# Performance work log

Hardware: AMD Instinct MI355X
Metric: run time of the kernel (lower is better)

Reference implementation:

```python
import jax, jax.numpy as jnp
import numpy as np
import math

N_COARSE, N_FINE = 8192, 32768
DEC_DIM, ENC_DIM, OUT_DIM, K = 256, 128, 128, 16
LN_EPS = 1e-5


def setup_inputs() -> dict:
    key = jax.random.key(0)
    ks = jax.random.split(key, 16)
    s = lambda fan_in: 1.0 / math.sqrt(fan_in)
    return {
        "decoder_features": jax.random.normal(ks[0], (N_COARSE, DEC_DIM), jnp.float32),
        "decoder_pos": jax.random.normal(ks[1], (N_COARSE, 3), jnp.float32),
        "encoder_features": jax.random.normal(ks[2], (N_FINE, ENC_DIM), jnp.float32),
        "encoder_pos": jax.random.normal(ks[3], (N_FINE, 3), jnp.float32),
        "encoder_labels": jax.random.randint(ks[4], (N_FINE,), 0, 13, jnp.int64),
        # params (torch nn.Linear default init scale)
        "Wq": jax.random.uniform(ks[5], (DEC_DIM, ENC_DIM), jnp.float32, -s(ENC_DIM), s(ENC_DIM)),
        "bq": jnp.zeros((DEC_DIM,), jnp.float32),
        "Wk": jax.random.uniform(ks[6], (DEC_DIM, DEC_DIM), jnp.float32, -s(DEC_DIM), s(DEC_DIM)),
        "bk": jnp.zeros((DEC_DIM,), jnp.float32),
        "Wv": jax.random.uniform(ks[7], (DEC_DIM, DEC_DIM), jnp.float32, -s(DEC_DIM), s(DEC_DIM)),
        "bv": jnp.zeros((DEC_DIM,), jnp.float32),
        "W1": jax.random.uniform(ks[8], (OUT_DIM, DEC_DIM + ENC_DIM), jnp.float32, -s(DEC_DIM + ENC_DIM), s(DEC_DIM + ENC_DIM)),
        "b1": jnp.zeros((OUT_DIM,), jnp.float32),
        "W2": jax.random.uniform(ks[9], (OUT_DIM, OUT_DIM), jnp.float32, -s(OUT_DIM), s(OUT_DIM)),
        "b2": jnp.zeros((OUT_DIM,), jnp.float32),
        "ln_g": jnp.ones((OUT_DIM,), jnp.float32),
        "ln_b": jnp.zeros((OUT_DIM,), jnp.float32),
    }


def _knn_indices(encoder_pos, decoder_pos, k):
    # For each fine (encoder) point, k nearest coarse (decoder) points.
    # squared distances [N_fine, N_coarse]
    d2 = (
        jnp.sum(encoder_pos * encoder_pos, axis=1, keepdims=True)
        - 2.0 * encoder_pos @ decoder_pos.T
        + jnp.sum(decoder_pos * decoder_pos, axis=1)[None, :]
    )
    _, idx = jax.lax.top_k(-d2, k)  # [N_fine, K]
    return idx


def reference(decoder_features, decoder_pos, encoder_features, encoder_pos,
              encoder_labels, Wq, bq, Wk, bk, Wv, bv, W1, b1, W2, b2, ln_g, ln_b):
    idx = _knn_indices(encoder_pos, decoder_pos, K)            # [Nf, K]
    nbr = decoder_features[idx]                                 # [Nf, K, Dd]
    query = encoder_features @ Wq.T + bq                        # [Nf, Dd]
    keys = nbr @ Wk.T + bk                                      # [Nf, K, Dd]
    values = nbr @ Wv.T + bv                                    # [Nf, K, Dd]
    scores = jnp.einsum('nd,nkd->nk', query, keys) / math.sqrt(DEC_DIM)
    # segment softmax over edges grouped by fine target == softmax over K
    weights = jax.nn.softmax(scores, axis=-1)                   # [Nf, K]
    agg = jnp.einsum('nk,nkd->nd', weights, values)             # [Nf, Dd]
    combined = jnp.concatenate([agg, encoder_features], axis=-1)
    h = jax.nn.relu(combined @ W1.T + b1)
    up = h @ W2.T + b2                                          # [Nf, out]
    mu = jnp.mean(up, axis=-1, keepdims=True)
    var = jnp.var(up, axis=-1, keepdims=True)
    out = (up - mu) * jax.lax.rsqrt(var + LN_EPS) * ln_g + ln_b
    # dropout is identity in eval mode
    return (out, encoder_pos, encoder_labels)
```

## Files before the change

kernel.cpp:

```cpp
#include <hip/hip_runtime.h>
#include <hip/hip_bf16.h>

typedef __hip_bfloat16 bf16;
typedef unsigned short u16;
typedef float f32x2 __attribute__((ext_vector_type(2)));

#define NC 8192
#define NF 32768
#define KNN 16
#define FMAXV 3.402823466e+38f

__device__ __forceinline__ float bfbits2f(u16 u){
  union { unsigned u; float f; } x; x.u = ((unsigned)u) << 16; return x.f;
}
__device__ __forceinline__ float asfloat(unsigned u){
  union { unsigned u; float f; } x; x.u = u; return x.f;
}
__device__ __forceinline__ f32x2 pk_fma(f32x2 a, f32x2 b, f32x2 c){
  f32x2 d;
  asm("v_pk_fma_f32 %0, %1, %2, %3" : "=v"(d) : "v"(a), "v"(b), "v"(c));
  return d;
}

__global__ __launch_bounds__(256) void k_prep(const float* __restrict__ dpos,
                                              const float* __restrict__ W1,
                                              const float* __restrict__ W2,
                                              float4* __restrict__ posP,
                                              float4* __restrict__ W1eSa,
                                              float4* __restrict__ W1eSb,
                                              float4* __restrict__ W2Sa,
                                              float4* __restrict__ W2Sb){
  int g = blockIdx.x * 256 + threadIdx.x;
  if (g < 4096){
    const float2* dp2 = (const float2*)(dpos + (size_t)g * 6);
    float2 a = dp2[0], b = dp2[1], c = dp2[2];
    float x0 = a.x, y0 = a.y, z0 = b.x;
    float x1 = b.y, y1 = c.x, z1 = c.y;
    float dd0 = __fadd_rn(__fadd_rn(__fmul_rn(x0,x0), __fmul_rn(y0,y0)), __fmul_rn(z0,z0));
    float dd1 = __fadd_rn(__fadd_rn(__fmul_rn(x1,x1), __fmul_rn(y1,y1)), __fmul_rn(z1,z1));
    posP[g * 2]     = make_float4(x0, x1, y0, y1);
    posP[g * 2 + 1] = make_float4(z0, z1, dd0 * 0.5f, dd1 * 0.5f);
  } else if (g >= 8192 && g < 10240){
    int f = g - 8192; int c4 = f >> 6, jg = f & 63;
    W1eSa[f] = ((const float4*)(W1 + (size_t)(2 * jg) * 384 + 256))[c4];
  } else if (g >= 10240 && g < 12288){
    int f = g - 10240; int c4 = f >> 6, jg = f & 63;
    W1eSb[f] = ((const float4*)(W1 + (size_t)(2 * jg + 1) * 384 + 256))[c4];
  } else if (g >= 12288 && g < 14336){
    int f = g - 12288; int c4 = f >> 6, jg = f & 63;
    W2Sa[f] = ((const float4*)(W2 + (size_t)(2 * jg) * 128))[c4];
  } else if (g >= 14336){
    int f = g - 14336; int c4 = f >> 6, jg = f & 63;
    W2Sb[f] = ((const float4*)(W2 + (size_t)(2 * jg + 1) * 128))[c4];
  }
}

__global__ __launch_bounds__(256) void k_wprod(const float* __restrict__ Wk,
                                               const float* __restrict__ Wv,
                                               const float* __restrict__ Wq,
                                               const float* __restrict__ W1,
                                               const float* __restrict__ bk,
                                               const float* __restrict__ bv,
                                               const float* __restrict__ bq,
                                               float* __restrict__ WkqS,
                                               float* __restrict__ WvuS,
                                               float* __restrict__ bkq,
                                               float* __restrict__ bvu,
                                               float* __restrict__ wbq,
                                               float* __restrict__ sbq){
  __shared__ float red[256];
  int b = blockIdx.x, t = threadIdx.x;
  if (b < 128){
    int c = b;
    float acc = 0.f;
    for (int j = 0; j < 256; ++j)
      acc = fmaf(Wk[(size_t)j * 256 + t], Wq[(size_t)j * 128 + c], acc);
    WkqS[(size_t)((t >> 2) * 128 + c) * 4 + (t & 3)] = acc;
    red[t] = bk[t] * Wq[(size_t)t * 128 + c];
    __syncthreads();
    for (int s = 128; s > 0; s >>= 1){ if (t < s) red[t] += red[t + s]; __syncthreads(); }
    if (t == 0) bkq[c] = red[0];
  } else if (b < 256){
    int h = b - 128;
    float acc = 0.f;
    for (int c2 = 0; c2 < 256; ++c2)
      acc = fmaf(Wv[(size_t)c2 * 256 + t], W1[(size_t)h * 384 + c2], acc);
    WvuS[(size_t)((t >> 2) * 128 + h) * 4 + (t & 3)] = acc;
    red[t] = bv[t] * W1[(size_t)h * 384 + t];
    __syncthreads();
    for (int s = 128; s > 0; s >>= 1){ if (t < s) red[t] += red[t + s]; __syncthreads(); }
    if (t == 0) bvu[h] = red[0];
  } else {
    float acc = 0.f;
    for (int j = 0; j < 256; ++j)
      acc = fmaf(Wk[(size_t)j * 256 + t], bq[j], acc);
    wbq[t] = acc;
    red[t] = bk[t] * bq[t];
    __syncthreads();
    for (int s = 128; s > 0; s >>= 1){ if (t < s) red[t] += red[t + s]; __syncthreads(); }
    if (t == 0) sbq[0] = red[0];
  }
}

__global__ __launch_bounds__(256) void k_dec(const float* __restrict__ df,
                                             const float4* __restrict__ WkqS,
                                             const float4* __restrict__ WvuS,
                                             const float* __restrict__ bkq,
                                             const float* __restrict__ bvu,
                                             const float* __restrict__ wbq,
                                             const float* __restrict__ sbq,
                                             bf16* __restrict__ Zd, bf16* __restrict__ Ud,
                                             float* __restrict__ bqK){
  __shared__ float part[16][16];
  int t = threadIdx.x;
  int g0 = blockIdx.x * 16;
  int half = __builtin_amdgcn_readfirstlane(t >> 7);
  int c = t & 127;
  const float4* W = half ? WvuS : WkqS;
  float acc[16];
  #pragma unroll
  for (int p = 0; p < 16; ++p) acc[p] = 0.f;
  for (int j4 = 0; j4 < 64; ++j4){
    float4 w = W[j4 * 128 + c];
    #pragma unroll
    for (int p = 0; p < 16; ++p){
      float4 a = ((const float4*)(df + (size_t)(g0 + p) * 256))[j4];
      acc[p] += w.x*a.x + w.y*a.y + w.z*a.z + w.w*a.w;
    }
  }
  float bias = half ? bvu[c] : bkq[c];
  bf16* dst = half ? Ud : Zd;
  #pragma unroll
  for (int p = 0; p < 16; ++p)
    dst[(size_t)(g0 + p) * 128 + c] = __float2bfloat16(acc[p] + bias);
  {
    int r = t >> 4, seg = t & 15;
    float s = 0.f;
    const float* dr = df + (size_t)(g0 + r) * 256 + seg * 16;
    const float* wq = wbq + seg * 16;
    #pragma unroll
    for (int e = 0; e < 16; ++e) s = fmaf(dr[e], wq[e], s);
    part[r][seg] = s;
  }
  __syncthreads();
  if (t < 16){
    float s = sbq[0];
    #pragma unroll
    for (int seg = 0; seg < 16; ++seg) s += part[t][seg];
    bqK[g0 + t] = s;
  }
}

__global__ __launch_bounds__(256) void k_attn(const float* __restrict__ epos,
                                              const float4* __restrict__ posP,
                                              const float* __restrict__ ef,
                                              const bf16* __restrict__ Zd,
                                              const bf16* __restrict__ Ud,
                                              const float* __restrict__ bqK,
                                              bf16* __restrict__ hagg){
  __shared__ float smin[8 * 64];
  __shared__ float tauLDS[8];
  __shared__ int   cnt[8];
  __shared__ float lval[8][64];
  __shared__ int   lidx[8][64];

  int t = threadIdx.x, lane = t & 63, w = t >> 6;
  int n0 = blockIdx.x * 8;
  f32x2 nex2[8], ney2[8], nez2[8];
  #pragma unroll
  for (int p = 0; p < 8; ++p){
    float nx = -epos[(n0 + p) * 3 + 0];
    float ny = -epos[(n0 + p) * 3 + 1];
    float nz = -epos[(n0 + p) * 3 + 2];
    nex2[p].x = nx; nex2[p].y = nx;
    ney2[p].x = ny; ney2[p].y = ny;
    nez2[p].x = nz; nez2[p].y = nz;
  }
  const float4* base = posP + w * 2048;

  f32x2 vmin2[8];
  #pragma unroll
  for (int p = 0; p < 8; ++p){ vmin2[p].x = FMAXV; vmin2[p].y = FMAXV; }
  #pragma unroll 2
  for (int s = 0; s < 16; ++s){
    int q2 = (s * 64 + lane) * 2;
    float4 XY = base[q2], ZW = base[q2 + 1];
    f32x2 X = {XY.x, XY.y}, Y = {XY.z, XY.w}, Z = {ZW.x, ZW.y}, W = {ZW.z, ZW.w};
    #pragma unroll
    for (int p = 0; p < 8; ++p){
      f32x2 v2 = pk_fma(nex2[p], X, W);
      v2 = pk_fma(ney2[p], Y, v2);
      v2 = pk_fma(nez2[p], Z, v2);
      vmin2[p].x = fminf(vmin2[p].x, v2.x);
      vmin2[p].y = fminf(vmin2[p].y, v2.y);
    }
  }
  float vmin[8];
  #pragma unroll
  for (int p = 0; p < 8; ++p) vmin[p] = fminf(vmin2[p].x, vmin2[p].y);

  #pragma unroll
  for (int k = 2; k <= 64; k <<= 1){
    #pragma unroll
    for (int j = k >> 1; j > 0; j >>= 1){
      bool keepmin = ((lane & j) == 0) == ((lane & k) == 0);
      #pragma unroll
      for (int p = 0; p < 8; ++p){
        float pv = __shfl_xor(vmin[p], j);
        vmin[p] = keepmin ? fminf(vmin[p], pv) : fmaxf(vmin[p], pv);
      }
    }
  }
  if (lane < 16){
    #pragma unroll
    for (int p = 0; p < 8; ++p) smin[p * 64 + w * 16 + lane] = vmin[p];
  }
  if (t < 8) cnt[t] = 0;
  __syncthreads();
  #pragma unroll
  for (int u = 0; u < 2; ++u){
    int p = w * 2 + u;
    float v = smin[p * 64 + lane];
    #pragma unroll
    for (int k = 2; k <= 64; k <<= 1){
      #pragma unroll
      for (int j = k >> 1; j > 0; j >>= 1){
        float pv = __shfl_xor(v, j);
        bool keepmin = ((lane & j) == 0) == ((lane & k) == 0);
        v = keepmin ? fminf(v, pv) : fmaxf(v, pv);
      }
    }
    if (lane == 16) tauLDS[p] = v;
  }
  __syncthreads();
  float tau0[8];
  #pragma unroll
  for (int p = 0; p < 8; ++p) tau0[p] = tauLDS[p];

  #pragma unroll 2
  for (int s = 0; s < 16; ++s){
    int q = s * 64 + lane;
    float4 XY = base[q * 2], ZW = base[q * 2 + 1];
    f32x2 X = {XY.x, XY.y}, Y = {XY.z, XY.w}, Z = {ZW.x, ZW.y}, W = {ZW.z, ZW.w};
    int cand0 = w * 2048 + q * 2;
    #pragma unroll
    for (int p = 0; p < 8; ++p){
      f32x2 v2 = pk_fma(nex2[p], X, W);
      v2 = pk_fma(ney2[p], Y, v2);
      v2 = pk_fma(nez2[p], Z, v2);
      if (v2.x <= tau0[p]){
        int slot = atomicAdd(&cnt[p], 1);
        if (slot < 64){ lval[p][slot] = v2.x; lidx[p][slot] = cand0; }
      }
      if (v2.y <= tau0[p]){
        int slot = atomicAdd(&cnt[p], 1);
        if (slot < 64){ lval[p][slot] = v2.y; lidx[p][slot] = cand0 + 1; }
      }
    }
  }
  __syncthreads();

  for (int u = 0; u < 2; ++u){
    int p = w * 2 + u;
    int n = n0 + p;
    int c = cnt[p]; if (c > 64) c = 64;
    float v  = (lane < c) ? lval[p][lane] : FMAXV;
    int   id = (lane < c) ? lidx[p][lane] : 0x7fffffff;
    #pragma unroll
    for (int k = 2; k <= 64; k <<= 1){
      #pragma unroll
      for (int j = k >> 1; j > 0; j >>= 1){
        float pv  = __shfl_xor(v, j);
        int   pid = __shfl_xor(id, j);
        bool keepmin = ((lane & j) == 0) == ((lane & k) == 0);
        bool pless = (pv < v) || (pv == v && pid < id);
        bool take = keepmin ? pless : !pless;
        if (take){ v = pv; id = pid; }
      }
    }
    int topi = id;

    *(float2*)&smin[w * 128 + lane * 2] = *(const float2*)(ef + (size_t)n * 128 + lane * 2);
    asm volatile("s_waitcnt lgkmcnt(0)" ::: "memory");

    int kk = lane & 15, part = lane >> 4;
    int ik = __shfl(topi, kk);
    const uint4*  zr = (const uint4*)((const u16*)Zd + (size_t)ik * 128) + part * 4;
    const float4* e4 = (const float4*)(smin + w * 128) + part * 8;
    float pr = 0.f;
    #pragma unroll
    for (int i = 0; i < 4; ++i){
      uint4 z = zr[i];
      float4 ea = e4[2 * i], eb = e4[2 * i + 1];
      pr = fmaf(ea.x, asfloat(z.x << 16), pr); pr = fmaf(ea.y, asfloat(z.x & 0xffff0000u), pr);
      pr = fmaf(ea.z, asfloat(z.y << 16), pr); pr = fmaf(ea.w, asfloat(z.y & 0xffff0000u), pr);
      pr = fmaf(eb.x, asfloat(z.z << 16), pr); pr = fmaf(eb.y, asfloat(z.z & 0xffff0000u), pr);
      pr = fmaf(eb.z, asfloat(z.w << 16), pr); pr = fmaf(eb.w, asfloat(z.w & 0xffff0000u), pr);
    }
    pr += __shfl_xor(pr, 16);
    pr += __shfl_xor(pr, 32);
    float sc = (pr + bqK[ik]) * (1.0f / 16.0f);

    float mx = sc;
    #pragma unroll
    for (int off = 8; off >= 1; off >>= 1) mx = fmaxf(mx, __shfl_xor(mx, off));
    float e = (lane < KNN) ? __expf(sc - mx) : 0.f;
    float l = e;
    #pragma unroll
    for (int off = 8; off >= 1; off >>= 1) l += __shfl_xor(l, off);
    float wgt = (lane < KNN) ? (e / l) : 0.f;

    float a0 = 0.f, a1 = 0.f;
    #pragma unroll
    for (int k = 0; k < KNN; ++k){
      int ikk = __shfl(topi, k);
      float wk = __shfl(wgt, k);
      ushort2 uu = *(const ushort2*)((const u16*)Ud + (size_t)ikk * 128 + lane * 2);
      a0 = fmaf(wk, bfbits2f(uu.x), a0);
      a1 = fmaf(wk, bfbits2f(uu.y), a1);
    }
    bf16 h0 = __float2bfloat16(a0), h1 = __float2bfloat16(a1);
    ushort2 st; st.x = *(u16*)&h0; st.y = *(u16*)&h1;
    *(ushort2*)(hagg + (size_t)n * 128 + lane * 2) = st;
  }
}

__global__ __launch_bounds__(256) void k_mlp(const bf16* __restrict__ hagg,
                                             const float* __restrict__ ef,
                                             const float4* __restrict__ W1eSa,
                                             const float4* __restrict__ W1eSb,
                                             const float* __restrict__ b1,
                                             const float4* __restrict__ W2Sa,
                                             const float4* __restrict__ W2Sb,
                                             const float* __restrict__ b2,
                                             const float* __restrict__ lng, const float* __restrict__ lnb,
                                             const float* __restrict__ epos, const int* __restrict__ lab,
                                             float* __restrict__ out){
  __shared__ float hbuf[16 * 128];
  __shared__ float ubuf[16 * 128];
  __shared__ float stats[32];
  int t = threadIdx.x;
  int n0 = blockIdx.x * 16;
  {
    int gid = blockIdx.x * 256 + t;
    if (gid < NF){
      float* op = out + (size_t)NF * 128;
      op[gid * 3 + 0] = epos[gid * 3 + 0];
      op[gid * 3 + 1] = epos[gid * 3 + 1];
      op[gid * 3 + 2] = epos[gid * 3 + 2];
      out[(size_t)NF * 128 + (size_t)NF * 3 + gid] = (float)lab[gid];
    }
  }
  int jg = t & 63;
  int pg4 = __builtin_amdgcn_readfirstlane((t >> 6) * 4);
  int j0 = jg * 2;
  float acc[2][4];
  #pragma unroll
  for (int a = 0; a < 2; ++a)
    #pragma unroll
    for (int p = 0; p < 4; ++p) acc[a][p] = 0.f;
  for (int c4 = 0; c4 < 32; ++c4){
    float4 wa = W1eSa[c4 * 64 + jg];
    float4 wb = W1eSb[c4 * 64 + jg];
    #pragma unroll
    for (int p = 0; p < 4; ++p){
      float4 x = ((const float4*)(ef + (size_t)(n0 + pg4 + p) * 128))[c4];
      acc[0][p] += wa.x*x.x + wa.y*x.y + wa.z*x.z + wa.w*x.w;
      acc[1][p] += wb.x*x.x + wb.y*x.y + wb.z*x.z + wb.w*x.w;
    }
  }
  float b1a = b1[j0], b1b = b1[j0 + 1];
  #pragma unroll
  for (int p = 0; p < 4; ++p){
    size_t row = (size_t)(n0 + pg4 + p);
    ushort2 hgv = *(const ushort2*)((const u16*)hagg + row * 128 + j0);
    hbuf[(pg4 + p) * 128 + j0]     = fmaxf(acc[0][p] + b1a + bfbits2f(hgv.x), 0.f);
    hbuf[(pg4 + p) * 128 + j0 + 1] = fmaxf(acc[1][p] + b1b + bfbits2f(hgv.y), 0.f);
  }
  __syncthreads();
  float acc2[2][4];
  #pragma unroll
  for (int a = 0; a < 2; ++a)
    #pragma unroll
    for (int p = 0; p < 4; ++p) acc2[a][p] = 0.f;
  const float4* hb4 = (const float4*)hbuf;
  for (int c4 = 0; c4 < 32; ++c4){
    float4 wa = W2Sa[c4 * 64 + jg];
    float4 wb = W2Sb[c4 * 64 + jg];
    #pragma unroll
    for (int p = 0; p < 4; ++p){
      float4 x = hb4[(pg4 + p) * 32 + c4];
      acc2[0][p] += wa.x*x.x + wa.y*x.y + wa.z*x.z + wa.w*x.w;
      acc2[1][p] += wb.x*x.x + wb.y*x.y + wb.z*x.z + wb.w*x.w;
    }
  }
  float b2a = b2[j0], b2b = b2[j0 + 1];
  float u[2][4];
  #pragma unroll
  for (int p = 0; p < 4; ++p){
    u[0][p] = acc2[0][p] + b2a;
    u[1][p] = acc2[1][p] + b2b;
    ubuf[(pg4 + p) * 128 + j0]     = u[0][p];
    ubuf[(pg4 + p) * 128 + j0 + 1] = u[1][p];
  }
  __syncthreads();
  {
    int p = t >> 4, qi = t & 15;
    const float* ub = &ubuf[p * 128 + qi * 8];
    float s = 0.f, s2 = 0.f;
    #pragma unroll
    for (int e2i = 0; e2i < 8; ++e2i){ float v = ub[e2i]; s += v; s2 += v * v; }
    #pragma unroll
    for (int off = 1; off < 16; off <<= 1){ s += __shfl_xor(s, off); s2 += __shfl_xor(s2, off); }
    if (qi == 0){
      float mu = s * (1.f / 128.f);
      float var = s2 * (1.f / 128.f) - mu * mu;
      stats[p] = mu;
      stats[16 + p] = rsqrtf(fmaxf(var, 0.f) + 1e-5f);
    }
  }
  __syncthreads();
  float ga = lng[j0], gb = lng[j0 + 1];
  float ba = lnb[j0], bbv = lnb[j0 + 1];
  #pragma unroll
  for (int p = 0; p < 4; ++p){
    float mu = stats[pg4 + p], rs = stats[16 + pg4 + p];
    out[(size_t)(n0 + pg4 + p) * 128 + j0]     = (u[0][p] - mu) * rs * ga + ba;
    out[(size_t)(n0 + pg4 + p) * 128 + j0 + 1] = (u[1][p] - mu) * rs * gb + bbv;
  }
}

extern "C" void kernel_launch(void* const* d_in, const int* in_sizes, int n_in,
                              void* d_out, int out_size, void* d_ws, size_t ws_size,
                              hipStream_t stream){
  const float* df   = (const float*)d_in[0];
  const float* dpos = (const float*)d_in[1];
  const float* ef   = (const float*)d_in[2];
  const float* epos = (const float*)d_in[3];
  const int*   lab  = (const int*)d_in[4];
  const float* Wq = (const float*)d_in[5];
  const float* bq = (const float*)d_in[6];
  const float* Wk = (const float*)d_in[7];
  const float* bk = (const float*)d_in[8];
  const float* Wv = (const float*)d_in[9];
  const float* bv = (const float*)d_in[10];
  const float* W1 = (const float*)d_in[11];
  const float* b1 = (const float*)d_in[12];
  const float* W2 = (const float*)d_in[13];
  const float* b2 = (const float*)d_in[14];
  const float* lng = (const float*)d_in[15];
  const float* lnb = (const float*)d_in[16];
  float* out = (float*)d_out;

  char* wsb = (char*)d_ws;
  float4* posP  = (float4*)(wsb);
  bf16*   Zd    = (bf16*)(wsb + 131072);
  bf16*   Ud    = (bf16*)(wsb + 2228224);
  float*  bqK   = (float*)(wsb + 4325376);
  bf16*   hagg  = (bf16*)(wsb + 4358144);
  float4* W1eSa = (float4*)(wsb + 12746752);
  float4* W1eSb = (float4*)(wsb + 12779520);
  float4* W2Sa  = (float4*)(wsb + 12812288);
  float4* W2Sb  = (float4*)(wsb + 12845056);
  float*  WkqS  = (float*)(wsb + 12877824);
  float*  WvuS  = (float*)(wsb + 13008896);
  float*  bkq   = (float*)(wsb + 13139968);
  float*  bvu   = (float*)(wsb + 13140480);
  float*  wbq   = (float*)(wsb + 13140992);
  float*  sbq   = (float*)(wsb + 13142016);

  k_prep  <<<64,  256, 0, stream>>>(dpos, W1, W2, posP, W1eSa, W1eSb, W2Sa, W2Sb);
  k_wprod <<<257, 256, 0, stream>>>(Wk, Wv, Wq, W1, bk, bv, bq, WkqS, WvuS, bkq, bvu, wbq, sbq);
  k_dec   <<<NC / 16, 256, 0, stream>>>(df, (const float4*)WkqS, (const float4*)WvuS, bkq, bvu, wbq, sbq, Zd, Ud, bqK);
  k_attn  <<<NF / 8, 256, 0, stream>>>(epos, posP, ef, Zd, Ud, bqK, hagg);
  k_mlp   <<<NF / 16, 256, 0, stream>>>(hagg, ef, W1eSa, W1eSb, b1, W2Sa, W2Sb, b2, lng, lnb, epos, lab, out);
  (void)in_sizes; (void)n_in; (void)out_size; (void)ws_size;
}
```

Before: 335.2 us.

## Interleave two query points per wave and shorten bitonic sorts in kNN kernel

Processes the two query points per wave together instead of in a sequential loop, interleaving shuffles, loads and FMAs to expose more instruction-level parallelism. The threshold selection builds a bitonic sequence from two pre-sorted 16-runs by mirrored indexing, so only merge stages are needed. The top-16 selection uses sort-16 then min-merge steps instead of a full 64-wide sort. The encoder feature row is read directly from global memory rather than staged through LDS. This raises register pressure and relies on the partial-sort logic being correct.

```diff
diff --git a/kernel.cpp b/kernel.cpp
--- a/kernel.cpp
+++ b/kernel.cpp
@@ -217,20 +217,24 @@
   }
   if (t < 8) cnt[t] = 0;
   __syncthreads();
-  #pragma unroll
-  for (int u = 0; u < 2; ++u){
-    int p = w * 2 + u;
-    float v = smin[p * 64 + lane];
-    #pragma unroll
-    for (int k = 2; k <= 64; k <<= 1){
-      #pragma unroll
-      for (int j = k >> 1; j > 0; j >>= 1){
-        float pv = __shfl_xor(v, j);
-        bool keepmin = ((lane & j) == 0) == ((lane & k) == 0);
-        v = keepmin ? fminf(v, pv) : fmaxf(v, pv);
-      }
-    }
-    if (lane == 16) tauLDS[p] = v;
+
+  {
+    int src = (lane & 16) ? (lane ^ 15) : lane;
+    float v0 = smin[(w * 2 + 0) * 64 + src];
+    float v1 = smin[(w * 2 + 1) * 64 + src];
+    #pragma unroll
+    for (int j = 16; j > 0; j >>= 1){
+      bool keepmin = ((lane & 32) == 0) == ((lane & j) == 0);
+      float p0 = __shfl_xor(v0, j); v0 = keepmin ? fminf(v0, p0) : fmaxf(v0, p0);
+      float p1 = __shfl_xor(v1, j); v1 = keepmin ? fminf(v1, p1) : fmaxf(v1, p1);
+    }
+    #pragma unroll
+    for (int j = 32; j > 0; j >>= 1){
+      bool keepmin = ((lane & j) == 0);
+      float p0 = __shfl_xor(v0, j); v0 = keepmin ? fminf(v0, p0) : fmaxf(v0, p0);
+      float p1 = __shfl_xor(v1, j); v1 = keepmin ? fminf(v1, p1) : fmaxf(v1, p1);
+    }
+    if (lane == 16){ tauLDS[w * 2] = v0; tauLDS[w * 2 + 1] = v1; }
   }
   __syncthreads();
   float tau0[8];
@@ -260,68 +264,113 @@
   }
   __syncthreads();
 
-  for (int u = 0; u < 2; ++u){
-    int p = w * 2 + u;
-    int n = n0 + p;
-    int c = cnt[p]; if (c > 64) c = 64;
-    float v  = (lane < c) ? lval[p][lane] : FMAXV;
-    int   id = (lane < c) ? lidx[p][lane] : 0x7fffffff;
-    #pragma unroll
-    for (int k = 2; k <= 64; k <<= 1){
+  {
+    int p0 = w * 2, p1 = w * 2 + 1;
+    int nA = n0 + p0, nB = n0 + p1;
+    int c0 = cnt[p0]; if (c0 > 64) c0 = 64;
+    int c1 = cnt[p1]; if (c1 > 64) c1 = 64;
+    float va = (lane < c0) ? lval[p0][lane] : FMAXV;
+    int   ia = (lane < c0) ? lidx[p0][lane] : 0x7fffffff;
+    float vb = (lane < c1) ? lval[p1][lane] : FMAXV;
+    int   ib = (lane < c1) ? lidx[p1][lane] : 0x7fffffff;
+
+    #pragma unroll
+    for (int k = 2; k <= 16; k <<= 1){
       #pragma unroll
       for (int j = k >> 1; j > 0; j >>= 1){
-        float pv  = __shfl_xor(v, j);
-        int   pid = __shfl_xor(id, j);
-        bool keepmin = ((lane & j) == 0) == ((lane & k) == 0);
-        bool pless = (pv < v) || (pv == v && pid < id);
-        bool take = keepmin ? pless : !pless;
-        if (take){ v = pv; id = pid; }
+        bool keepmin = ((lane & k) == 0) == ((lane & j) == 0);
+        { float pv = __shfl_xor(va, j); int pid = __shfl_xor(ia, j);
+          bool pl = (pv < va) || (pv == va && pid < ia);
+          if (keepmin ? pl : !pl){ va = pv; ia = pid; } }
+        { float pv = __shfl_xor(vb, j); int pid = __shfl_xor(ib, j);
+          bool pl = (pv < vb) || (pv == vb && pid < ib);
+          if (keepmin ? pl : !pl){ vb = pv; ib = pid; } }
       }
     }
-    int topi = id;
-
-    *(float2*)&smin[w * 128 + lane * 2] = *(const float2*)(ef + (size_t)n * 128 + lane * 2);
-    asm volatile("s_waitcnt lgkmcnt(0)" ::: "memory");
+    { float pv = __shfl_xor(va, 16); int pid = __shfl_xor(ia, 16);
+      if ((pv < va) || (pv == va && pid < ia)){ va = pv; ia = pid; } }
+    { float pv = __shfl_xor(vb, 16); int pid = __shfl_xor(ib, 16);
+      if ((pv < vb) || (pv == vb && pid < ib)){ vb = pv; ib = pid; } }
+    #pragma unroll
+    for (int j = 8; j > 0; j >>= 1){
+      bool keepmin = ((lane & 32) == 0) == ((lane & j) == 0);
+      { float pv = __shfl_xor(va, j); int pid = __shfl_xor(ia, j);
+        bool pl = (pv < va) || (pv == va && pid < ia);
+        if (keepmin ? pl : !pl){ va = pv; ia = pid; } }
+      { float pv = __shfl_xor(vb, j); int pid = __shfl_xor(ib, j);
+        bool pl = (pv < vb) || (pv == vb && pid < ib);
+        if (keepmin ? pl : !pl){ vb = pv; ib = pid; } }
+    }
+    { float pv = __shfl_xor(va, 32); int pid = __shfl_xor(ia, 32);
+      if ((pv < va) || (pv == va && pid < ia)){ va = pv; ia = pid; } }
+    { float pv = __shfl_xor(vb, 32); int pid = __shfl_xor(ib, 32);
+      if ((pv < vb) || (pv == vb && pid < ib)){ vb = pv; ib = pid; } }
+    int topi0 = ia, topi1 = ib;
 
     int kk = lane & 15, part = lane >> 4;
-    int ik = __shfl(topi, kk);
-    const uint4*  zr = (const uint4*)((const u16*)Zd + (size_t)ik * 128) + part * 4;
-    const float4* e4 = (const float4*)(smin + w * 128) + part * 8;
-    float pr = 0.f;
+    int ik0 = __shfl(topi0, kk);
+    int ik1 = __shfl(topi1, kk);
+    const uint4*  zr0 = (const uint4*)((const u16*)Zd + (size_t)ik0 * 128) + part * 4;
+    const uint4*  zr1 = (const uint4*)((const u16*)Zd + (size_t)ik1 * 128) + part * 4;
+    const float4* e40 = (const float4*)(ef + (size_t)nA * 128) + part * 8;
+    const float4* e41 = (const float4*)(ef + (size_t)nB * 128) + part * 8;
+    float pr0 = 0.f, pr1 = 0.f;
     #pragma unroll
     for (int i = 0; i < 4; ++i){
-      uint4 z = zr[i];
-      float4 ea = e4[2 * i], eb = e4[2 * i + 1];
-      pr = fmaf(ea.x, asfloat(z.x << 16), pr); pr = fmaf(ea.y, asfloat(z.x & 0xffff0000u), pr);
-      pr = fmaf(ea.z, asfloat(z.y << 16), pr); pr = fmaf(ea.w, asfloat(z.y & 0xffff0000u), pr);
-      pr = fmaf(eb.x, asfloat(z.z << 16), pr); pr = fmaf(eb.y, asfloat(z.z & 0xffff0000u), pr);
-      pr = fmaf(eb.z, asfloat(z.w << 16), pr); pr = fmaf(eb.w, asfloat(z.w & 0xffff0000u), pr);
-    }
-    pr += __shfl_xor(pr, 16);
-    pr += __shfl_xor(pr, 32);
-    float sc = (pr + bqK[ik]) * (1.0f / 16.0f);
-
-    float mx = sc;
-    #pragma unroll
-    for (int off = 8; off >= 1; off >>= 1) mx = fmaxf(mx, __shfl_xor(mx, off));
-    float e = (lane < KNN) ? __expf(sc - mx) : 0.f;
-    float l = e;
-    #pragma unroll
-    for (int off = 8; off >= 1; off >>= 1) l += __shfl_xor(l, off);
-    float wgt = (lane < KNN) ? (e / l) : 0.f;
-
-    float a0 = 0.f, a1 = 0.f;
+      uint4 z0 = zr0[i], z1 = zr1[i];
+      float4 ea0 = e40[2 * i], eb0 = e40[2 * i + 1];
+      float4 ea1 = e41[2 * i], eb1 = e41[2 * i + 1];
+      pr0 = fmaf(ea0.x, asfloat(z0.x << 16), pr0); pr0 = fmaf(ea0.y, asfloat(z0.x & 0xffff0000u), pr0);
+      pr0 = fmaf(ea0.z, asfloat(z0.y << 16), pr0); pr0 = fmaf(ea0.w, asfloat(z0.y & 0xffff0000u), pr0);
+      pr0 = fmaf(eb0.x, asfloat(z0.z << 16), pr0); pr0 = fmaf(eb0.y, asfloat(z0.z & 0xffff0000u), pr0);
+      pr0 = fmaf(eb0.z, asfloat(z0.w << 16), pr0); pr0 = fmaf(eb0.w, asfloat(z0.w & 0xffff0000u), pr0);
+      pr1 = fmaf(ea1.x, asfloat(z1.x << 16), pr1); pr1 = fmaf(ea1.y, asfloat(z1.x & 0xffff0000u), pr1);
+      pr1 = fmaf(ea1.z, asfloat(z1.y << 16), pr1); pr1 = fmaf(ea1.w, asfloat(z1.y & 0xffff0000u), pr1);
+      pr1 = fmaf(eb1.x, asfloat(z1.z << 16), pr1); pr1 = fmaf(eb1.y, asfloat(z1.z & 0xffff0000u), pr1);
+      pr1 = fmaf(eb1.z, asfloat(z1.w << 16), pr1); pr1 = fmaf(eb1.w, asfloat(z1.w & 0xffff0000u), pr1);
+    }
+    pr0 += __shfl_xor(pr0, 16); pr1 += __shfl_xor(pr1, 16);
+    pr0 += __shfl_xor(pr0, 32); pr1 += __shfl_xor(pr1, 32);
+    float sc0 = (pr0 + bqK[ik0]) * (1.0f / 16.0f);
+    float sc1 = (pr1 + bqK[ik1]) * (1.0f / 16.0f);
+
+    float mx0 = sc0, mx1 = sc1;
+    #pragma unroll
+    for (int off = 8; off >= 1; off >>= 1){
+      mx0 = fmaxf(mx0, __shfl_xor(mx0, off));
+      mx1 = fmaxf(mx1, __shfl_xor(mx1, off));
+    }
+    float e0 = (lane < KNN) ? __expf(sc0 - mx0) : 0.f;
+    float e1 = (lane < KNN) ? __expf(sc1 - mx1) : 0.f;
+    float l0 = e0, l1 = e1;
+    #pragma unroll
+    for (int off = 8; off >= 1; off >>= 1){
+      l0 += __shfl_xor(l0, off);
+      l1 += __shfl_xor(l1, off);
+    }
+    float wgt0 = (lane < KNN) ? (e0 / l0) : 0.f;
+    float wgt1 = (lane < KNN) ? (e1 / l1) : 0.f;
+
+    float a00 = 0.f, a01 = 0.f, a10 = 0.f, a11 = 0.f;
     #pragma unroll
     for (int k = 0; k < KNN; ++k){
-      int ikk = __shfl(topi, k);
-      float wk = __shfl(wgt, k);
-      ushort2 uu = *(const ushort2*)((const u16*)Ud + (size_t)ikk * 128 + lane * 2);
-      a0 = fmaf(wk, bfbits2f(uu.x), a0);
-      a1 = fmaf(wk, bfbits2f(uu.y), a1);
-    }
-    bf16 h0 = __float2bfloat16(a0), h1 = __float2bfloat16(a1);
-    ushort2 st; st.x = *(u16*)&h0; st.y = *(u16*)&h1;
-    *(ushort2*)(hagg + (size_t)n * 128 + lane * 2) = st;
+      int ikk0 = __shfl(topi0, k);
+      int ikk1 = __shfl(topi1, k);
+      float wk0 = __shfl(wgt0, k);
+      float wk1 = __shfl(wgt1, k);
+      ushort2 u0 = *(const ushort2*)((const u16*)Ud + (size_t)ikk0 * 128 + lane * 2);
+      ushort2 u1 = *(const ushort2*)((const u16*)Ud + (size_t)ikk1 * 128 + lane * 2);
+      a00 = fmaf(wk0, bfbits2f(u0.x), a00);
+      a01 = fmaf(wk0, bfbits2f(u0.y), a01);
+      a10 = fmaf(wk1, bfbits2f(u1.x), a10);
+      a11 = fmaf(wk1, bfbits2f(u1.y), a11);
+    }
+    bf16 h00 = __float2bfloat16(a00), h01 = __float2bfloat16(a01);
+    bf16 h10 = __float2bfloat16(a10), h11 = __float2bfloat16(a11);
+    ushort2 st0; st0.x = *(u16*)&h00; st0.y = *(u16*)&h01;
+    ushort2 st1; st1.x = *(u16*)&h10; st1.y = *(u16*)&h11;
+    *(ushort2*)(hagg + (size_t)nA * 128 + lane * 2) = st0;
+    *(ushort2*)(hagg + (size_t)nB * 128 + lane * 2) = st1;
   }
 }
 
```

After: 339.2 us. About the same (+1.2%).
